# Kernel optimization log

Hardware: AMD Instinct MI355X
Metric: run time of the kernel (lower is better)

The kernel has to match this reference:

```python
import jax, jax.numpy as jnp
import numpy as np
import math

D_MODEL = 1024
LAYER_ID = 6
NUM_LAYERS = 12
B = 8
T = 2048


def setup_inputs() -> dict:
    key = jax.random.key(0)
    ks = jax.random.split(key, 5)
    r01 = LAYER_ID / (NUM_LAYERS - 1)
    r1a0 = 1.0 - LAYER_ID / NUM_LAYERS
    h = np.arange(D_MODEL, dtype=np.float32)
    w = (-5.0 + 8.0 * (h / (D_MODEL - 1)) ** (0.7 + 1.3 * r01)).astype(np.float32)
    zigzag = np.array([(i + 1) % 3 - 1 for i in range(D_MODEL)], np.float32) * 0.5
    u = (np.ones(D_MODEL, np.float32) * math.log(0.3) + zigzag).astype(np.float32)
    xinit = (h / D_MODEL).astype(np.float32)
    tmk = (xinit ** r1a0).reshape(1, 1, D_MODEL).astype(np.float32)
    tmv = (tmk + 0.3 * r01).astype(np.float32)
    tmr = (xinit ** (0.5 * r1a0)).reshape(1, 1, D_MODEL).astype(np.float32)
    s = 1.0 / math.sqrt(D_MODEL)
    Wk = jax.random.normal(ks[0], (D_MODEL, D_MODEL), jnp.float32) * s
    Wv = jax.random.normal(ks[1], (D_MODEL, D_MODEL), jnp.float32) * s
    Wr = jax.random.normal(ks[2], (D_MODEL, D_MODEL), jnp.float32) * s
    Wo = jax.random.normal(ks[3], (D_MODEL, D_MODEL), jnp.float32) * s
    x = jax.random.normal(ks[4], (B, T, D_MODEL), jnp.float32)
    return dict(
        x=x,
        w=jnp.asarray(w), u=jnp.asarray(u),
        time_mix_k=jnp.asarray(tmk), time_mix_v=jnpp if False else jnp.asarray(tmv), time_mix_r=jnp.asarray(tmr),
        Wk=Wk, Wv=Wv, Wr=Wr, Wo=Wo,
    )


def _wkv(w, u, k, v):
    # w,u: [C] (raw params); k,v: [B,T,C]. Numerically-stable RWKV scan.
    wn = -jnp.exp(w)  # decay (negative)

    def step(carry, kv):
        aa, bb, pp = carry  # each [B,C]
        kt, vt = kv         # [B,C]
        ww = u + kt
        p = jnp.maximum(pp, ww)
        e1 = jnp.exp(pp - p)
        e2 = jnp.exp(ww - p)
        y = (e1 * aa + e2 * vt) / (e1 * bb + e2)
        ww2 = pp + wn
        p2 = jnp.maximum(ww2, kt)
        e1b = jnp.exp(ww2 - p2)
        e2b = jnp.exp(kt - p2)
        return (e1b * aa + e2b * vt, e1b * bb + e2b, p2), y

    Bd, Td, Cd = k.shape
    init = (jnp.zeros((Bd, Cd), k.dtype), jnp.zeros((Bd, Cd), k.dtype),
            jnp.full((Bd, Cd), -1e38, k.dtype))
    kT = jnp.swapaxes(k, 0, 1)  # [T,B,C]
    vT = jnp.swapaxes(v, 0, 1)
    _, ys = jax.lax.scan(step, init, (kT, vT))
    return jnp.swapaxes(ys, 0, 1)  # [B,T,C]


def reference(x, w, u, time_mix_k, time_mix_v, time_mix_r, Wk, Wv, Wr, Wo):
    # token shift: zero-pad one step at the front of time, drop last
    xs = jnp.pad(x, ((0, 0), (1, 0), (0, 0)))[:, :-1]
    xk = x * time_mix_k + xs * (1.0 - time_mix_k)
    xv = x * time_mix_v + xs * (1.0 - time_mix_v)
    xr = x * time_mix_r + xs * (1.0 - time_mix_r)
    k = jnp.einsum('btc,dc->btd', xk, Wk)
    v = jnp.einsum('btc,dc->btd', xv, Wv)
    r = jnp.einsum('btc,dc->btd', xr, Wr)
    wkv = _wkv(w, u, k, v)
    rwkv = jax.nn.sigmoid(r) * wkv
    return jnp.einsum('btc,dc->btd', rwkv, Wo)
```

## Files before the change

### kernel.cpp

```cpp
#include <hip/hip_runtime.h>
#include <hip/hip_bf16.h>
#include <stdint.h>

#define DM     1024
#define BATCH  8
#define SEQ    2048
#define MROWS  (BATCH * SEQ)
#define NCH    32
#define NCHL2  5
#define CHL    (SEQ / NCH)
#define NT     (DM / 64)

typedef unsigned short u16;
typedef __attribute__((ext_vector_type(8))) __bf16 bf16x8;
typedef __attribute__((ext_vector_type(4))) float  f32x4;

#define MB (1024ull * 1024ull)

__device__ __forceinline__ u16 f2bf(float f) {
    unsigned u = __float_as_uint(f);
    u += 0x7fffu + ((u >> 16) & 1u);
    return (u16)(u >> 16);
}
__device__ __forceinline__ float bf2f(u16 h) {
    return __uint_as_float(((unsigned)h) << 16);
}

__device__ __forceinline__ bool in_f32(const void* wraw) {
    return ((*(const unsigned*)wraw) & 0xFFFFu) == 0u;
}

__device__ __forceinline__ void ld16_lds(const u16* g, u16* l) {
    __builtin_amdgcn_global_load_lds(
        (const __attribute__((address_space(1))) void*)g,
        (__attribute__((address_space(3))) void*)l, 16, 0, 0);
}

__global__ __launch_bounds__(256) void mix_stream(
    const void* __restrict__ xraw,
    const void* __restrict__ tmkraw,
    const void* __restrict__ tmvraw,
    const void* __restrict__ tmrraw,
    const void* __restrict__ wraw,
    u16* __restrict__ xk, u16* __restrict__ xv, u16* __restrict__ xr)
{
    const bool f32i = in_f32(wraw);
    const int tid = threadIdx.x;
    const int c4  = tid << 2;

    float mk[4], mv[4], mr[4];
    if (f32i) {
        #pragma unroll
        for (int j = 0; j < 4; ++j) {
            mk[j] = ((const float*)tmkraw)[c4 + j];
            mv[j] = ((const float*)tmvraw)[c4 + j];
            mr[j] = ((const float*)tmrraw)[c4 + j];
        }
    } else {
        union { u16 h[4]; uint2 u; } a, b, c;
        a.u = *(const uint2*)((const u16*)tmkraw + c4);
        b.u = *(const uint2*)((const u16*)tmvraw + c4);
        c.u = *(const uint2*)((const u16*)tmrraw + c4);
        #pragma unroll
        for (int j = 0; j < 4; ++j) {
            mk[j] = bf2f(a.h[j]); mv[j] = bf2f(b.h[j]); mr[j] = bf2f(c.h[j]);
        }
    }

    #pragma unroll
    for (int it = 0; it < 8; ++it) {
        const int r = blockIdx.x + (it << 11);
        const size_t o = (size_t)r * DM + c4;
        const bool first = (r & (SEQ - 1)) == 0;

        float xf[4], sf[4];
        if (f32i) {
            f32x4 a = *(const f32x4*)((const float*)xraw + o);
            #pragma unroll
            for (int j = 0; j < 4; ++j) xf[j] = a[j];
            if (first) {
                #pragma unroll
                for (int j = 0; j < 4; ++j) sf[j] = 0.f;
            } else {
                f32x4 s = *(const f32x4*)((const float*)xraw + o - DM);
                #pragma unroll
                for (int j = 0; j < 4; ++j) sf[j] = s[j];
            }
        } else {
            union { u16 h[4]; uint2 u; } a, s;
            a.u = *(const uint2*)((const u16*)xraw + o);
            #pragma unroll
            for (int j = 0; j < 4; ++j) xf[j] = bf2f(a.h[j]);
            if (first) {
                #pragma unroll
                for (int j = 0; j < 4; ++j) sf[j] = 0.f;
            } else {
                s.u = *(const uint2*)((const u16*)xraw + o - DM);
                #pragma unroll
                for (int j = 0; j < 4; ++j) sf[j] = bf2f(s.h[j]);
            }
        }

        union { u16 h[4]; uint2 u; } ok, ov, orr;
        #pragma unroll
        for (int j = 0; j < 4; ++j) {
            float d = xf[j] - sf[j];
            ok.h[j]  = f2bf(sf[j] + mk[j] * d);
            ov.h[j]  = f2bf(sf[j] + mv[j] * d);
            orr.h[j] = f2bf(sf[j] + mr[j] * d);
        }
        *(uint2*)(xk + o) = ok.u;
        *(uint2*)(xv + o) = ov.u;
        *(uint2*)(xr + o) = orr.u;
    }
}

__global__ __launch_bounds__(256) void cast_w4(
    const void* __restrict__ W0, const void* __restrict__ W1,
    const void* __restrict__ W2, const void* __restrict__ W3,
    const void* __restrict__ wflag,
    u16* __restrict__ o0, u16* __restrict__ o1,
    u16* __restrict__ o2, u16* __restrict__ o3)
{
    const void* Ws[4] = {W0, W1, W2, W3};
    u16*        os[4] = {o0, o1, o2, o3};
    const void* Wraw = Ws[blockIdx.y];
    u16*        Wb   = os[blockIdx.y];
    int i = (blockIdx.x * 256 + threadIdx.x) << 2;
    if (in_f32(wflag)) {
        float4 wv = *(const float4*)((const float*)Wraw + i);
        union { u16 h[4]; uint2 u; } p;
        p.h[0] = f2bf(wv.x); p.h[1] = f2bf(wv.y);
        p.h[2] = f2bf(wv.z); p.h[3] = f2bf(wv.w);
        *(uint2*)(Wb + i) = p.u;
    } else {
        *(uint2*)(Wb + i) = *(const uint2*)((const u16*)Wraw + i);
    }
}

template <int NZ>
__global__ __launch_bounds__(512) void gemm_bt(
    const u16* __restrict__ A0, const u16* __restrict__ A1, const u16* __restrict__ A2,
    const u16* __restrict__ B0, const u16* __restrict__ B1, const u16* __restrict__ B2,
    void* __restrict__ C0, void* __restrict__ C1, void* __restrict__ C2,
    int c0f32)
{
    __shared__ u16 As[2][256 * 64];
    __shared__ u16 Bs[2][256 * 64];

    const int lin = blockIdx.x;
    const int xcd = lin & 7;
    const int idx = lin >> 3;
    const int z   = idx >> 5;
    const int r   = idx & 31;
    const int bxe = r & 3;
    const int bye = xcd + ((r >> 2) << 3);

    const u16* __restrict__ A = (z == 0) ? A0 : (z == 1) ? A1 : A2;
    const u16* __restrict__ B = (z == 0) ? B0 : (z == 1) ? B1 : B2;
    void*      C = (z == 0) ? C0 : (z == 1) ? C1 : C2;
    const bool f32out = (z == 0) && c0f32;

    const int tid  = threadIdx.x;
    const int w    = tid >> 6, lane = tid & 63;
    const int wm   = w >> 2, wn = w & 3;
    const int lr   = lane & 15, quad = lane >> 4;
    const int tm   = bye * 256, tn = bxe * 256;

    const int srow = lane >> 3;
    const int scol = ((lane & 7) ^ srow) * 8;
    const u16* srcA = A + (size_t)(tm + srow) * DM + scol;
    const u16* srcB = B + (size_t)(tn + srow) * DM + scol;

    const int sw0 = (quad * 8) ^ ((lr & 7) * 8);
    const int sw1 = (32 + quad * 8) ^ ((lr & 7) * 8);
    const int arowb = (wm * 128 + lr) * 64;
    const int browb = (wn * 64 + lr) * 64;

    f32x4 acc[8][4] = {};

    auto stageA = [&](int t, int j) {
        int row = j * 64 + w * 8;
        ld16_lds(srcA + (size_t)row * DM + t * 64, &As[t & 1][row * 64]);
    };
    auto stageB = [&](int t, int j) {
        int row = j * 64 + w * 8;
        ld16_lds(srcB + (size_t)row * DM + t * 64, &Bs[t & 1][row * 64]);
    };

    #pragma unroll
    for (int j = 0; j < 4; ++j) stageA(0, j);
    #pragma unroll
    for (int j = 0; j < 4; ++j) stageB(0, j);
    #pragma unroll
    for (int j = 0; j < 4; ++j) stageA(1, j);
    asm volatile("s_waitcnt vmcnt(4)" ::: "memory");
    __builtin_amdgcn_s_barrier();

    bf16x8 af[4], bfr[4];

#define MFMA_BLOCK(MI0)                                                       \
    __builtin_amdgcn_s_barrier();                                             \
    __builtin_amdgcn_s_setprio(1);                                            \
    _Pragma("unroll")                                                         \
    for (int mi = 0; mi < 4; ++mi)                                            \
        _Pragma("unroll")                                                     \
        for (int ni = 0; ni < 4; ++ni)                                        \
            acc[MI0 + mi][ni] = __builtin_amdgcn_mfma_f32_16x16x32_bf16(      \
                af[mi], bfr[ni], acc[MI0 + mi][ni], 0, 0, 0);                 \
    __builtin_amdgcn_s_setprio(0);                                            \
    __builtin_amdgcn_s_barrier();

    #pragma unroll 2
    for (int t = 0; t < NT; ++t) {
        const u16* __restrict__ Ab = As[t & 1];
        const u16* __restrict__ Bb = Bs[t & 1];

        #pragma unroll
        for (int mi = 0; mi < 4; ++mi)
            af[mi] = *(const bf16x8*)&Ab[arowb + mi * 1024 + sw0];
        #pragma unroll
        for (int ni = 0; ni < 4; ++ni)
            bfr[ni] = *(const bf16x8*)&Bb[browb + ni * 1024 + sw0];
        if (t + 1 < NT) { stageB(t + 1, 0); stageB(t + 1, 1); }
        MFMA_BLOCK(0)

        #pragma unroll
        for (int mi = 0; mi < 4; ++mi)
            af[mi] = *(const bf16x8*)&Ab[arowb + 4096 + mi * 1024 + sw0];
        if (t + 1 < NT) { stageB(t + 1, 2); stageB(t + 1, 3); }
        MFMA_BLOCK(4)

        #pragma unroll
        for (int mi = 0; mi < 4; ++mi)
            af[mi] = *(const bf16x8*)&Ab[arowb + mi * 1024 + sw1];
        #pragma unroll
        for (int ni = 0; ni < 4; ++ni)
            bfr[ni] = *(const bf16x8*)&Bb[browb + ni * 1024 + sw1];
        MFMA_BLOCK(0)

        #pragma unroll
        for (int mi = 0; mi < 4; ++mi)
            af[mi] = *(const bf16x8*)&Ab[arowb + 4096 + mi * 1024 + sw1];
        if (t + 2 < NT) {
            #pragma unroll
            for (int j = 0; j < 4; ++j) stageA(t + 2, j);
            asm volatile("s_waitcnt vmcnt(4)" ::: "memory");
        } else {
            asm volatile("s_waitcnt vmcnt(0)" ::: "memory");
        }
        MFMA_BLOCK(4)
    }
#undef MFMA_BLOCK

    #pragma unroll
    for (int mi = 0; mi < 8; ++mi)
        #pragma unroll
        for (int ni = 0; ni < 4; ++ni)
            #pragma unroll
            for (int rr = 0; rr < 4; ++rr) {
                int row = tm + wm * 128 + mi * 16 + quad * 4 + rr;
                int col = tn + wn * 64 + ni * 16 + lr;
                float v = acc[mi][ni][rr];
                if (f32out) ((float*)C)[(size_t)row * DM + col] = v;
                else        ((u16*)C)[(size_t)row * DM + col]   = f2bf(v);
            }
}

__device__ __forceinline__ float ldval(const float* p) { return *p; }
__device__ __forceinline__ float ldval(const u16*  p) { return bf2f(*p); }

template <typename KT>
__global__ __launch_bounds__(256) void wkv_phase1(
    const KT* __restrict__ kk, const u16* __restrict__ vv,
    const void* __restrict__ wraw,
    float* __restrict__ sa, float* __restrict__ sb, float* __restrict__ sp)
{
    const int gid = blockIdx.x * 256 + threadIdx.x;
    const int c   = gid & (DM - 1);
    const int ch  = (gid >> 10) & (NCH - 1);
    const int b   = gid >> (10 + NCHL2);
    float wc = in_f32(wraw) ? ((const float*)wraw)[c] : bf2f(((const u16*)wraw)[c]);
    const float wn = -__expf(wc);

    const size_t base = ((size_t)b * SEQ + (size_t)ch * CHL) * DM + c;
    float la = 0.f, lb = 0.f, lp = -1e38f;

    float kb[8], vb[8];
    #pragma unroll
    for (int j = 0; j < 8; ++j) {
        size_t id = base + (size_t)j * DM;
        kb[j] = ldval(kk + id); vb[j] = ldval(vv + id);
    }
    for (int t0 = 0; t0 < CHL; t0 += 8) {
        const bool more = (t0 + 8) < CHL;
        float kn[8], vn[8];
        if (more) {
            size_t nb = base + (size_t)(t0 + 8) * DM;
            #pragma unroll
            for (int j = 0; j < 8; ++j) {
                size_t id = nb + (size_t)j * DM;
                kn[j] = ldval(kk + id); vn[j] = ldval(vv + id);
            }
        }
        #pragma unroll
        for (int j = 0; j < 8; ++j) {
            const float kt = kb[j], vt = vb[j];
            const float w2 = lp + wn;
            const float p2 = fmaxf(w2, kt);
            const float e1 = __expf(w2 - p2);
            const float e2 = __expf(kt - p2);
            la = e1 * la + e2 * vt;
            lb = e1 * lb + e2;
            lp = p2;
        }
        if (more) {
            #pragma unroll
            for (int j = 0; j < 8; ++j) { kb[j] = kn[j]; vb[j] = vn[j]; }
        }
    }
    const int sidx = ((b * NCH + ch) << 10) + c;
    sa[sidx] = la; sb[sidx] = lb; sp[sidx] = lp;
}

template <typename KT>
__global__ __launch_bounds__(256) void wkv_phase3(
    const KT* __restrict__ kk, const u16* __restrict__ vv,
    const u16* __restrict__ rr,
    const float* __restrict__ sa, const float* __restrict__ sb,
    const float* __restrict__ sp,
    const void* __restrict__ wraw, const void* __restrict__ uraw,
    u16* __restrict__ out)
{
    const int gid = blockIdx.x * 256 + threadIdx.x;
    const int c   = gid & (DM - 1);
    const int ch  = (gid >> 10) & (NCH - 1);
    const int b   = gid >> (10 + NCHL2);
    float wc, uc;
    if (in_f32(wraw)) {
        wc = ((const float*)wraw)[c]; uc = ((const float*)uraw)[c];
    } else {
        wc = bf2f(((const u16*)wraw)[c]); uc = bf2f(((const u16*)uraw)[c]);
    }
    const float wn = -__expf(wc);
    const float uu = uc;

    const float lamL = wn * (float)CHL;
    float aa = 0.f, bb = 0.f, pp = -1e38f;
    #pragma unroll 8
    for (int j = 0; j < ch; ++j) {
        const int idx = ((b * NCH + j) << 10) + c;
        const float la = sa[idx], lb = sb[idx], lp = sp[idx];
        const float w2 = pp + lamL;
        const float np = fmaxf(w2, lp);
        const float e1 = __expf(w2 - np);
        const float e2 = __expf(lp - np);
        aa = e1 * aa + e2 * la;
        bb = e1 * bb + e2 * lb;
        pp = np;
    }

    const size_t base = ((size_t)b * SEQ + (size_t)ch * CHL) * DM + c;

    float kb[8], vb[8], rb[8];
    #pragma unroll
    for (int j = 0; j < 8; ++j) {
        size_t id = base + (size_t)j * DM;
        kb[j] = ldval(kk + id); vb[j] = ldval(vv + id); rb[j] = ldval(rr + id);
    }
    for (int t0 = 0; t0 < CHL; t0 += 8) {
        const bool more = (t0 + 8) < CHL;
        float kn[8], vn[8], rn[8];
        if (more) {
            size_t nb = base + (size_t)(t0 + 8) * DM;
            #pragma unroll
            for (int j = 0; j < 8; ++j) {
                size_t id = nb + (size_t)j * DM;
                kn[j] = ldval(kk + id); vn[j] = ldval(vv + id); rn[j] = ldval(rr + id);
            }
        }
        #pragma unroll
        for (int j = 0; j < 8; ++j) {
            const float kt = kb[j], vt = vb[j], rt = rb[j];
            const float ww = uu + kt;
            const float p  = fmaxf(pp, ww);
            const float e1 = __expf(pp - p);
            const float e2 = __expf(ww - p);
            const float y  = (e1 * aa + e2 * vt) / (e1 * bb + e2);
            const float w2 = pp + wn;
            const float p2 = fmaxf(w2, kt);
            const float e1b = __expf(w2 - p2);
            const float e2b = __expf(kt - p2);
            aa = e1b * aa + e2b * vt;
            bb = e1b * bb + e2b;
            pp = p2;
            const float sr = 1.f / (1.f + __expf(-rt));
            out[base + (size_t)(t0 + j) * DM] = f2bf(sr * y);
        }
        if (more) {
            #pragma unroll
            for (int j = 0; j < 8; ++j) { kb[j] = kn[j]; vb[j] = vn[j]; rb[j] = rn[j]; }
        }
    }
}

extern "C" void kernel_launch(void* const* d_in, const int* in_sizes, int n_in,
                              void* d_out, int out_size, void* d_ws, size_t ws_size,
                              hipStream_t stream)
{
    const void* x   = d_in[0];
    const void* w   = d_in[1];
    const void* u   = d_in[2];
    const void* tmk = d_in[3];
    const void* tmv = d_in[4];
    const void* tmr = d_in[5];
    const void* Wk  = d_in[6];
    const void* Wv  = d_in[7];
    const void* Wr  = d_in[8];
    const void* Wo  = d_in[9];

    char* base = (char*)d_ws;
    const bool kf32 = ws_size >= 168 * MB;
    u16* Wkb  = (u16*)(base);
    u16* Wvb  = (u16*)(base + 2 * MB);
    u16* Wrb  = (u16*)(base + 4 * MB);
    u16* Wob  = (u16*)(base + 6 * MB);
    u16* xk   = (u16*)(base + 8 * MB);
    u16* xv   = (u16*)(base + 40 * MB);
    u16* xr   = (u16*)(base + 72 * MB);
    void* kbuf = (void*)(base + 104 * MB);
    u16* vb   = xk;
    u16* rb   = xv;
    u16* rwkv = xr;
    float* sa   = (float*)(base);
    float* sbuf = (float*)(base + 1 * MB);
    float* sp   = (float*)(base + 2 * MB);

    cast_w4<<<dim3(DM * DM / 1024, 4), 256, 0, stream>>>(
        Wk, Wv, Wr, Wo, w, Wkb, Wvb, Wrb, Wob);
    mix_stream<<<2048, 256, 0, stream>>>(x, tmk, tmv, tmr, w, xk, xv, xr);

    gemm_bt<3><<<768, 512, 0, stream>>>(
        xk, xv, xr, Wkb, Wvb, Wrb, kbuf, vb, rb, kf32 ? 1 : 0);

    const int scan_threads = BATCH * NCH * DM;
    if (kf32) {
        wkv_phase1<float><<<scan_threads / 256, 256, 0, stream>>>(
            (const float*)kbuf, vb, w, sa, sbuf, sp);
        wkv_phase3<float><<<scan_threads / 256, 256, 0, stream>>>(
            (const float*)kbuf, vb, rb, sa, sbuf, sp, w, u, rwkv);
    } else {
        wkv_phase1<u16><<<scan_threads / 256, 256, 0, stream>>>(
            (const u16*)kbuf, vb, w, sa, sbuf, sp);
        wkv_phase3<u16><<<scan_threads / 256, 256, 0, stream>>>(
            (const u16*)kbuf, vb, rb, sa, sbuf, sp, w, u, rwkv);
    }

    gemm_bt<1><<<256, 512, 0, stream>>>(
        rwkv, rwkv, rwkv, Wob, Wob, Wob, d_out, d_out, d_out, 1);
}
```

Measured before the change: 356.9 us.

## Fuse WKV chunk scan phases with inter-block flags and merge prep kernels

```diff
diff --git a/kernel.cpp b/kernel.cpp
--- a/kernel.cpp
+++ b/kernel.cpp
@@ -36,17 +36,55 @@
         (__attribute__((address_space(3))) void*)l, 16, 0, 0);
 }
 
-__global__ __launch_bounds__(256) void mix_stream(
+__device__ __forceinline__ void st_coh(float* p, float v) {
+    __hip_atomic_store(p, v, __ATOMIC_RELAXED, __HIP_MEMORY_SCOPE_AGENT);
+}
+__device__ __forceinline__ float ld_coh(const float* p) {
+    return __hip_atomic_load(p, __ATOMIC_RELAXED, __HIP_MEMORY_SCOPE_AGENT);
+}
+
+__global__ __launch_bounds__(256) void prep(
     const void* __restrict__ xraw,
     const void* __restrict__ tmkraw,
     const void* __restrict__ tmvraw,
     const void* __restrict__ tmrraw,
     const void* __restrict__ wraw,
-    u16* __restrict__ xk, u16* __restrict__ xv, u16* __restrict__ xr)
+    const void* __restrict__ W0, const void* __restrict__ W1,
+    const void* __restrict__ W2, const void* __restrict__ W3,
+    u16* __restrict__ o0, u16* __restrict__ o1,
+    u16* __restrict__ o2, u16* __restrict__ o3,
+    u16* __restrict__ xk, u16* __restrict__ xv, u16* __restrict__ xr,
+    int* __restrict__ flags)
 {
     const bool f32i = in_f32(wraw);
     const int tid = threadIdx.x;
-    const int c4  = tid << 2;
+    const int bx  = blockIdx.x;
+
+    if (blockIdx.y != 0) {
+        const void* Ws[4] = {W0, W1, W2, W3};
+        u16*        os[4] = {o0, o1, o2, o3};
+        const int m = (blockIdx.y - 1) * 2 + (bx >> 10);
+        const void* Wraw = Ws[m];
+        u16*        Wb   = os[m];
+        int i = ((bx & 1023) * 256 + tid) << 2;
+        if (f32i) {
+            float4 wv = *(const float4*)((const float*)Wraw + i);
+            union { u16 h[4]; uint2 u; } p;
+            p.h[0] = f2bf(wv.x); p.h[1] = f2bf(wv.y);
+            p.h[2] = f2bf(wv.z); p.h[3] = f2bf(wv.w);
+            *(uint2*)(Wb + i) = p.u;
+        } else {
+            *(uint2*)(Wb + i) = *(const uint2*)((const u16*)Wraw + i);
+        }
+        return;
+    }
+
+    if (bx == 0) {
+        #pragma unroll
+        for (int i = 0; i < 4; ++i) flags[tid * 4 + i] = 0;
+    }
+
+    const int c4 = tid << 2;
 
     float mk[4], mv[4], mr[4];
     if (f32i) {
@@ -69,7 +107,7 @@
 
     #pragma unroll
     for (int it = 0; it < 8; ++it) {
-        const int r = blockIdx.x + (it << 11);
+        const int r = bx + (it << 11);
         const size_t o = (size_t)r * DM + c4;
         const bool first = (r & (SEQ - 1)) == 0;
 
@@ -112,29 +150,6 @@
         *(uint2*)(xk + o) = ok.u;
         *(uint2*)(xv + o) = ov.u;
         *(uint2*)(xr + o) = orr.u;
-    }
-}
-
-__global__ __launch_bounds__(256) void cast_w4(
-    const void* __restrict__ W0, const void* __restrict__ W1,
-    const void* __restrict__ W2, const void* __restrict__ W3,
-    const void* __restrict__ wflag,
-    u16* __restrict__ o0, u16* __restrict__ o1,
-    u16* __restrict__ o2, u16* __restrict__ o3)
-{
-    const void* Ws[4] = {W0, W1, W2, W3};
-    u16*        os[4] = {o0, o1, o2, o3};
-    const void* Wraw = Ws[blockIdx.y];
-    u16*        Wb   = os[blockIdx.y];
-    int i = (blockIdx.x * 256 + threadIdx.x) << 2;
-    if (in_f32(wflag)) {
-        float4 wv = *(const float4*)((const float*)Wraw + i);
-        union { u16 h[4]; uint2 u; } p;
-        p.h[0] = f2bf(wv.x); p.h[1] = f2bf(wv.y);
-        p.h[2] = f2bf(wv.z); p.h[3] = f2bf(wv.w);
-        *(uint2*)(Wb + i) = p.u;
-    } else {
-        *(uint2*)(Wb + i) = *(const uint2*)((const u16*)Wraw + i);
     }
 }
 
@@ -271,71 +286,21 @@
 __device__ __forceinline__ float ldval(const u16*  p) { return bf2f(*p); }
 
 template <typename KT>
-__global__ __launch_bounds__(256) void wkv_phase1(
-    const KT* __restrict__ kk, const u16* __restrict__ vv,
-    const void* __restrict__ wraw,
-    float* __restrict__ sa, float* __restrict__ sb, float* __restrict__ sp)
-{
-    const int gid = blockIdx.x * 256 + threadIdx.x;
-    const int c   = gid & (DM - 1);
-    const int ch  = (gid >> 10) & (NCH - 1);
-    const int b   = gid >> (10 + NCHL2);
-    float wc = in_f32(wraw) ? ((const float*)wraw)[c] : bf2f(((const u16*)wraw)[c]);
-    const float wn = -__expf(wc);
-
-    const size_t base = ((size_t)b * SEQ + (size_t)ch * CHL) * DM + c;
-    float la = 0.f, lb = 0.f, lp = -1e38f;
-
-    float kb[8], vb[8];
-    #pragma unroll
-    for (int j = 0; j < 8; ++j) {
-        size_t id = base + (size_t)j * DM;
-        kb[j] = ldval(kk + id); vb[j] = ldval(vv + id);
-    }
-    for (int t0 = 0; t0 < CHL; t0 += 8) {
-        const bool more = (t0 + 8) < CHL;
-        float kn[8], vn[8];
-        if (more) {
-            size_t nb = base + (size_t)(t0 + 8) * DM;
-            #pragma unroll
-            for (int j = 0; j < 8; ++j) {
-                size_t id = nb + (size_t)j * DM;
-                kn[j] = ldval(kk + id); vn[j] = ldval(vv + id);
-            }
-        }
-        #pragma unroll
-        for (int j = 0; j < 8; ++j) {
-            const float kt = kb[j], vt = vb[j];
-            const float w2 = lp + wn;
-            const float p2 = fmaxf(w2, kt);
-            const float e1 = __expf(w2 - p2);
-            const float e2 = __expf(kt - p2);
-            la = e1 * la + e2 * vt;
-            lb = e1 * lb + e2;
-            lp = p2;
-        }
-        if (more) {
-            #pragma unroll
-            for (int j = 0; j < 8; ++j) { kb[j] = kn[j]; vb[j] = vn[j]; }
-        }
-    }
-    const int sidx = ((b * NCH + ch) << 10) + c;
-    sa[sidx] = la; sb[sidx] = lb; sp[sidx] = lp;
-}
-
-template <typename KT>
-__global__ __launch_bounds__(256) void wkv_phase3(
+__global__ __launch_bounds__(256, 4) void wkv_fused(
     const KT* __restrict__ kk, const u16* __restrict__ vv,
     const u16* __restrict__ rr,
-    const float* __restrict__ sa, const float* __restrict__ sb,
-    const float* __restrict__ sp,
+    float* __restrict__ sa, float* __restrict__ sb, float* __restrict__ sp,
     const void* __restrict__ wraw, const void* __restrict__ uraw,
-    u16* __restrict__ out)
+    u16* __restrict__ out, int* __restrict__ flags)
 {
-    const int gid = blockIdx.x * 256 + threadIdx.x;
+    const int bx  = blockIdx.x;
+    const int tid = threadIdx.x;
+    const int gid = bx * 256 + tid;
     const int c   = gid & (DM - 1);
-    const int ch  = (gid >> 10) & (NCH - 1);
-    const int b   = gid >> (10 + NCHL2);
+    const int ch  = (bx >> 2) & (NCH - 1);
+    const int b   = bx >> 7;
+    const int cblk = bx & 3;
+
     float wc, uc;
     if (in_f32(wraw)) {
         wc = ((const float*)wraw)[c]; uc = ((const float*)uraw)[c];
@@ -345,22 +310,85 @@
     const float wn = -__expf(wc);
     const float uu = uc;
 
+    const size_t base = ((size_t)b * SEQ + (size_t)ch * CHL) * DM + c;
+
+    {
+        float la = 0.f, lb = 0.f, lp = -1e38f;
+        float kb[8], vb[8];
+        #pragma unroll
+        for (int j = 0; j < 8; ++j) {
+            size_t id = base + (size_t)j * DM;
+            kb[j] = ldval(kk + id); vb[j] = ldval(vv + id);
+        }
+        for (int t0 = 0; t0 < CHL; t0 += 8) {
+            const bool more = (t0 + 8) < CHL;
+            float kn[8], vn[8];
+            if (more) {
+                size_t nb = base + (size_t)(t0 + 8) * DM;
+                #pragma unroll
+                for (int j = 0; j < 8; ++j) {
+                    size_t id = nb + (size_t)j * DM;
+                    kn[j] = ldval(kk + id); vn[j] = ldval(vv + id);
+                }
+            }
+            #pragma unroll
+            for (int j = 0; j < 8; ++j) {
+                const float kt = kb[j], vt = vb[j];
+                const float w2 = lp + wn;
+                const float p2 = fmaxf(w2, kt);
+                const float e1 = __expf(w2 - p2);
+                const float e2 = __expf(kt - p2);
+                la = e1 * la + e2 * vt;
+                lb = e1 * lb + e2;
+                lp = p2;
+            }
+            if (more) {
+                #pragma unroll
+                for (int j = 0; j < 8; ++j) { kb[j] = kn[j]; vb[j] = vn[j]; }
+            }
+        }
+        const int sidx = ((b * NCH + ch) << 10) + c;
+        st_coh(&sa[sidx], la); st_coh(&sb[sidx], lb); st_coh(&sp[sidx], lp);
+    }
+    __syncthreads();
+    if (tid == 0)
+        __hip_atomic_store(&flags[bx], 1, __ATOMIC_RELAXED,
+                           __HIP_MEMORY_SCOPE_AGENT);
+
+    if (tid < ch) {
+        const int pidx = (b << 7) | (tid << 2) | cblk;
+        while (__hip_atomic_load(&flags[pidx], __ATOMIC_RELAXED,
+                                 __HIP_MEMORY_SCOPE_AGENT) == 0)
+            __builtin_amdgcn_s_sleep(2);
+    }
+    __syncthreads();
+
     const float lamL = wn * (float)CHL;
     float aa = 0.f, bb = 0.f, pp = -1e38f;
-    #pragma unroll 8
-    for (int j = 0; j < ch; ++j) {
-        const int idx = ((b * NCH + j) << 10) + c;
-        const float la = sa[idx], lb = sb[idx], lp = sp[idx];
-        const float w2 = pp + lamL;
-        const float np = fmaxf(w2, lp);
-        const float e1 = __expf(w2 - np);
-        const float e2 = __expf(lp - np);
-        aa = e1 * aa + e2 * la;
-        bb = e1 * bb + e2 * lb;
-        pp = np;
-    }
-
-    const size_t base = ((size_t)b * SEQ + (size_t)ch * CHL) * DM + c;
+    #pragma unroll 1
+    for (int j0 = 0; j0 < ch; j0 += 8) {
+        float la8[8], lb8[8], lp8[8];
+        #pragma unroll
+        for (int q = 0; q < 8; ++q) {
+            int jj = j0 + q; if (jj >= ch) jj = j0;
+            const int idx = ((b * NCH + jj) << 10) + c;
+            la8[q] = ld_coh(&sa[idx]);
+            lb8[q] = ld_coh(&sb[idx]);
+            lp8[q] = ld_coh(&sp[idx]);
+        }
+        #pragma unroll
+        for (int q = 0; q < 8; ++q) {
+            if (j0 + q < ch) {
+                const float w2 = pp + lamL;
+                const float np = fmaxf(w2, lp8[q]);
+                const float e1 = __expf(w2 - np);
+                const float e2 = __expf(lp8[q] - np);
+                aa = e1 * aa + e2 * la8[q];
+                bb = e1 * bb + e2 * lb8[q];
+                pp = np;
+            }
+        }
+    }
 
     float kb[8], vb[8], rb[8];
     #pragma unroll
@@ -435,25 +463,22 @@
     float* sa   = (float*)(base);
     float* sbuf = (float*)(base + 1 * MB);
     float* sp   = (float*)(base + 2 * MB);
-
-    cast_w4<<<dim3(DM * DM / 1024, 4), 256, 0, stream>>>(
-        Wk, Wv, Wr, Wo, w, Wkb, Wvb, Wrb, Wob);
-    mix_stream<<<2048, 256, 0, stream>>>(x, tmk, tmv, tmr, w, xk, xv, xr);
+    int* flags = (int*)d_out;
+
+    prep<<<dim3(2048, 3), 256, 0, stream>>>(
+        x, tmk, tmv, tmr, w,
+        Wk, Wv, Wr, Wo, Wkb, Wvb, Wrb, Wob, xk, xv, xr, flags);
 
     gemm_bt<3><<<768, 512, 0, stream>>>(
         xk, xv, xr, Wkb, Wvb, Wrb, kbuf, vb, rb, kf32 ? 1 : 0);
 
-    const int scan_threads = BATCH * NCH * DM;
+    const int scan_blocks = BATCH * NCH * DM / 256;
     if (kf32) {
-        wkv_phase1<float><<<scan_threads / 256, 256, 0, stream>>>(
-            (const float*)kbuf, vb, w, sa, sbuf, sp);
-        wkv_phase3<float><<<scan_threads / 256, 256, 0, stream>>>(
-            (const float*)kbuf, vb, rb, sa, sbuf, sp, w, u, rwkv);
+        wkv_fused<float><<<scan_blocks, 256, 0, stream>>>(
+            (const float*)kbuf, vb, rb, sa, sbuf, sp, w, u, rwkv, flags);
     } else {
-        wkv_phase1<u16><<<scan_threads / 256, 256, 0, stream>>>(
-            (const u16*)kbuf, vb, w, sa, sbuf, sp);
-        wkv_phase3<u16><<<scan_threads / 256, 256, 0, stream>>>(
-            (const u16*)kbuf, vb, rb, sa, sbuf, sp, w, u, rwkv);
+        wkv_fused<u16><<<scan_blocks, 256, 0, stream>>>(
+            (const u16*)kbuf, vb, rb, sa, sbuf, sp, w, u, rwkv, flags);
     }
 
     gemm_bt<1><<<256, 512, 0, stream>>>(
```

Result: no change. 359.8 us (+0.8%).
